# Kernel tuning notes

Hardware: AMD Instinct MI355X
Metric: run time of the kernel (lower is better)

## Reference

```python
import jax, jax.numpy as jnp
import numpy as np

B, OBS, ACT_DIM, C, CTX, H = 128, 512, 7, 100, 128, 512
IN = OBS + 1 + CTX  # states + scalar action component + context = 641


def cont2disc(values, n):
    return jnp.clip(jnp.floor((values + 1.0) / 2.0 * n), 0, n - 1)


def setup_inputs() -> dict:
    key = jax.random.key(0)
    ks = jax.random.split(key, 10)
    def w(k, shape):
        return jax.random.normal(k, shape, dtype=jnp.float32) / np.sqrt(shape[-2])
    return {
        "observations": jax.random.normal(ks[0], (B, OBS), dtype=jnp.float32),
        "actions": jax.random.uniform(ks[1], (B, ACT_DIM), dtype=jnp.float32, minval=-1.0, maxval=1.0),
        # one MLP per action dim (weight_sharing=False): layers IN->H->H->CTX
        "W1": w(ks[2], (ACT_DIM, IN, H)),  "b1": jnp.zeros((ACT_DIM, H), jnp.float32),
        "W2": w(ks[3], (ACT_DIM, H, H)),   "b2": jnp.zeros((ACT_DIM, H), jnp.float32),
        "W3": w(ks[4], (ACT_DIM, H, CTX)), "b3": jnp.zeros((ACT_DIM, CTX), jnp.float32),
        # output_proj = MLP((1,)): single dense CTX->1, no activation
        "Wp": w(ks[5], (CTX, 1)), "bp": jnp.zeros((1,), jnp.float32),
        "compute_lse": 1,
    }


def reference(observations, actions, W1, b1, W2, b2, W3, b3, Wp, bp, compute_lse):
    n = observations.shape[0]
    acts = cont2disc(actions, C)  # [B, ACT_DIM], float component indices
    context = jnp.zeros((n, CTX), observations.dtype)
    comp = jnp.arange(C, dtype=observations.dtype)  # candidate components 0..C-1
    q = jnp.zeros((n, ACT_DIM * C), observations.dtype)

    for i in range(1, ACT_DIM):
        def mlp(x, i=i):  # hidden layers relu, final layer linear
            h = jax.nn.relu(x @ W1[i] + b1[i])
            h = jax.nn.relu(h @ W2[i] + b2[i])
            return h @ W3[i] + b3[i]

        # batched over all num_components candidate actions (replaces the per-j loop)
        xin = jnp.concatenate([
            jnp.broadcast_to(observations[:, None, :], (n, C, OBS)),
            jnp.broadcast_to(comp[None, :, None], (n, C, 1)),
            jnp.broadcast_to(context[:, None, :], (n, C, CTX)),
        ], axis=-1)  # [B, C, IN]
        curr_ctx = mlp(xin) + context[:, None, :]        # [B, C, CTX]
        qv = (curr_ctx @ Wp + bp)[..., 0]                # [B, C]
        q = q.at[:, (i - 1) * C : i * C].set(qv)          # which_qval ordering

        # advance context with the actual (discretized) action
        x = jnp.concatenate([observations, acts[:, i:i + 1], context], axis=-1)
        context = mlp(x) + context

    if compute_lse:
        return jax.scipy.special.logsumexp(q, axis=-1)    # [B]
    return context @ Wp + bp                              # [B, 1]
```

## Files before the change

### kernel.cpp

```cpp
#include <hip/hip_runtime.h>
#include <math.h>

#define BATCH 128
#define ACT 7
#define NC 100
#define CTXD 128
#define HID 512
#define QW 600

typedef __attribute__((ext_vector_type(8))) __bf16 bf16x8;
typedef __attribute__((ext_vector_type(4))) float f32x4;
typedef __attribute__((ext_vector_type(4))) unsigned short u16x4;

__device__ __forceinline__ unsigned short f2bf(float f) {
    union { float f; unsigned int u; } v; v.f = f;
    unsigned int u = v.u;
    return (unsigned short)((u + 0x7fffu + ((u >> 16) & 1u)) >> 16);
}
__device__ __forceinline__ unsigned int pack2bf(float a, float b) {
    unsigned int ua = __float_as_uint(a) + 0x8000u;
    unsigned int ub = __float_as_uint(b) + 0x8000u;
    return (ua >> 16) | (ub & 0xffff0000u);
}

__device__ __forceinline__ void async16(const void* g, void* l) {
    __builtin_amdgcn_global_load_lds(
        (const __attribute__((address_space(1))) unsigned int*)(uintptr_t)g,
        (__attribute__((address_space(3))) unsigned int*)(unsigned int)(uintptr_t)l,
        16, 0, 0);
}

__global__ void prep_kernel(const float* __restrict__ obs, const float* __restrict__ W1,
                            const float* __restrict__ W2, const float* __restrict__ W3,
                            const float* __restrict__ Wp,
                            unsigned short* __restrict__ obs_bf, unsigned short* __restrict__ W1Cbf,
                            unsigned short* __restrict__ W2bf, unsigned short* __restrict__ W3bf,
                            unsigned short* __restrict__ W1AT, unsigned short* __restrict__ W2T,
                            float* __restrict__ vq) {
    const int bidx = blockIdx.x, tid = threadIdx.x;
    if (bidx < 2368) {
        const int e = (bidx * 256 + tid) * 4;
        const float* src; unsigned short* dst;
        if (e < 65536)        { src = obs + e; dst = obs_bf + e; }
        else if (e < 458752)  { int f = e - 65536; int i = f >> 16; int rem = f & 65535;
                                src = W1 + (size_t)(i + 1) * 328192 + 513*512 + rem; dst = W1Cbf + f; }
        else if (e < 2031616) { int f = e - 458752; src = W2 + 262144 + f; dst = W2bf + f; }
        else                  { int f = e - 2031616; src = W3 + 65536 + f; dst = W3bf + f; }
        float4 v = *(const float4*)src;
        u16x4 o; o[0] = f2bf(v.x); o[1] = f2bf(v.y); o[2] = f2bf(v.z); o[3] = f2bf(v.w);
        *(u16x4*)dst = o;
    } else if (bidx < 5440) {
        __shared__ float tile[32][33];
        const int idx = bidx - 2368;
        const int z = idx >> 8, rem = idx & 255;
        const int rb = rem & 15, cb = rem >> 4;
        const float* ip; unsigned short* op;
        if (z < 6) { ip = W1 + (size_t)(z + 1) * 328192; op = W1AT + (size_t)z * 262144; }
        else       { int i = z - 6; ip = W2 + (size_t)(i + 1) * 262144; op = W2T + (size_t)i * 262144; }
        const int r0 = rb * 32, c0 = cb * 32;
        const int tx = tid & 31, ty = tid >> 5;
        #pragma unroll
        for (int j = 0; j < 32; j += 8)
            tile[ty + j][tx] = ip[(size_t)(r0 + ty + j) * 512 + c0 + tx];
        __syncthreads();
        #pragma unroll
        for (int j = 0; j < 32; j += 8)
            op[(size_t)(c0 + ty + j) * 512 + r0 + tx] = f2bf(tile[tx][ty + j]);
    } else {
        const int idx = bidx - 5440;
        const int z = idx >> 1, k = (idx & 1) * 256 + tid;
        const float4* row = (const float4*)(W3 + (size_t)(z + 1) * 65536 + (size_t)k * 128);
        const float4* wp4 = (const float4*)Wp;
        float s = 0.f;
        #pragma unroll 8
        for (int n = 0; n < 32; ++n) {
            float4 a = row[n], w = wp4[n];
            s += a.x*w.x + a.y*w.y + a.z*w.z + a.w*w.w;
        }
        vq[z * 512 + k] = s;
    }
}

__launch_bounds__(256)
__global__ void yobs_kernel(const unsigned short* __restrict__ A,
                            const unsigned short* __restrict__ BtAll,
                            const float* __restrict__ b1,
                            float* __restrict__ Yobs) {
    __shared__ unsigned short As[64*32];
    __shared__ unsigned short Bs[128*32];
    const int m0 = blockIdx.x * 64;
    const int n0 = blockIdx.y * 128;
    const int z  = blockIdx.z;
    const unsigned short* Bt = BtAll + (size_t)z * 262144;
    const int tid = threadIdx.x, lane = tid & 63, wave = tid >> 6;
    const int wm = wave >> 1, wn = wave & 1;
    const int srow = tid >> 2, skc = (tid & 3) * 8;
    const unsigned short* gA  = A  + (size_t)(m0 + srow) * HID + skc;
    const unsigned short* gB0 = Bt + (size_t)(n0 + srow) * HID + skc;
    const unsigned short* gB1 = gB0 + 64 * HID;
    f32x4 acc[2][4] = {};
    for (int k0 = 0; k0 < HID; k0 += 32) {
        async16(gA + k0, As + tid*8);
        async16(gB0 + k0, Bs + tid*8);
        async16(gB1 + k0, Bs + 2048 + tid*8);
        __syncthreads();
        const int q8 = (lane >> 4) * 8, l15 = lane & 15;
        bf16x8 af[2], bfr[4];
        #pragma unroll
        for (int mt = 0; mt < 2; ++mt)
            af[mt] = *(const bf16x8*)(As + (wm*32 + mt*16 + l15) * 32 + q8);
        #pragma unroll
        for (int nt = 0; nt < 4; ++nt)
            bfr[nt] = *(const bf16x8*)(Bs + (wn*64 + nt*16 + l15) * 32 + q8);
        #pragma unroll
        for (int mt = 0; mt < 2; ++mt)
            #pragma unroll
            for (int nt = 0; nt < 4; ++nt)
                acc[mt][nt] = __builtin_amdgcn_mfma_f32_16x16x32_bf16(af[mt], bfr[nt], acc[mt][nt], 0, 0, 0);
        __syncthreads();
    }
    const int colL = wn*64 + (lane & 15);
    #pragma unroll
    for (int nt = 0; nt < 4; ++nt) {
        const int col = n0 + colL + nt*16;
        const float bb = b1[(z + 1) * HID + col];
        #pragma unroll
        for (int mt = 0; mt < 2; ++mt)
            #pragma unroll
            for (int r = 0; r < 4; ++r) {
                const int row = m0 + wm*32 + mt*16 + (lane >> 4)*4 + r;
                Yobs[(size_t)z * 65536 + (size_t)row * HID + col] = acc[mt][nt][r] + bb;
            }
    }
}

__launch_bounds__(1024)
__global__ void chain_kernel(const float* __restrict__ Yobs, const float* __restrict__ W1,
                             const unsigned short* __restrict__ W1Cbf,
                             const unsigned short* __restrict__ W2bf,
                             const unsigned short* __restrict__ W3bf,
                             const float* __restrict__ b2, const float* __restrict__ b3,
                             const float* __restrict__ actions,
                             const float* __restrict__ Wp, const float* __restrict__ bp,
                             float* __restrict__ Y0all, float* __restrict__ QOFF) {
    const int b = blockIdx.x, t = threadIdx.x;
    __shared__ float ctx[128], h1[512], h2s[512];
    __shared__ float part[2048];
    const int pair = t & 255, kq = t >> 8;
    const int pair3 = t & 63, kq3 = t >> 6;
    if (t < 128) ctx[t] = 0.f;
    __syncthreads();
    for (int i = 1; i <= 6; ++i) {
        if (t < 128) part[t] = (ctx[t] + b3[i*128 + t]) * Wp[t];
        __syncthreads();
        if (t < 64) {
            float v = part[t] + part[t + 64];
            #pragma unroll
            for (int o = 32; o > 0; o >>= 1) v += __shfl_down(v, o, 64);
            if (t == 0) QOFF[(i-1)*128 + b] = v + bp[0];
        }
        __syncthreads();
        const float a = actions[b*ACT + i];
        float fj = floorf((a + 1.0f) * 50.0f);
        fj = fminf(fmaxf(fj, 0.0f), 99.0f);
        {
            const unsigned int* wp1 = (const unsigned int*)(W1Cbf + (size_t)(i-1)*65536) + pair;
            float acc0 = 0.f, acc1 = 0.f;
            #pragma unroll 8
            for (int k = kq*32; k < kq*32 + 32; ++k) {
                unsigned int u = wp1[k*256];
                float c = ctx[k];
                acc0 = fmaf(c, __uint_as_float(u << 16), acc0);
                acc1 = fmaf(c, __uint_as_float(u & 0xffff0000u), acc1);
            }
            *(float2*)(&part[kq*512 + 2*pair]) = make_float2(acc0, acc1);
        }
        __syncthreads();
        if (t < 256) {
            const int n2 = 2*t;
            float2 p0 = *(const float2*)(&part[n2]);
            float2 p1 = *(const float2*)(&part[512 + n2]);
            float2 p2 = *(const float2*)(&part[1024 + n2]);
            float2 p3 = *(const float2*)(&part[1536 + n2]);
            float2 yo = *(const float2*)(Yobs + (size_t)(i-1)*65536 + b*512 + n2);
            float y0a = yo.x + p0.x + p1.x + p2.x + p3.x;
            float y0b = yo.y + p0.y + p1.y + p2.y + p3.y;
            *(float2*)(Y0all + (size_t)(i-1)*65536 + b*512 + n2) = make_float2(y0a, y0b);
            const float* w1a = W1 + (size_t)i*328192 + 262144;
            float2 wv = *(const float2*)(w1a + n2);
            h1[n2]   = fmaxf(fmaf(fj, wv.x, y0a), 0.f);
            h1[n2+1] = fmaxf(fmaf(fj, wv.y, y0b), 0.f);
        }
        __syncthreads();
        {
            const unsigned int* wp2 = (const unsigned int*)(W2bf + (size_t)(i-1)*262144) + pair;
            float acc0 = 0.f, acc1 = 0.f;
            #pragma unroll 16
            for (int k = kq*128; k < kq*128 + 128; ++k) {
                unsigned int u = wp2[k*256];
                float hv = h1[k];
                acc0 = fmaf(hv, __uint_as_float(u << 16), acc0);
                acc1 = fmaf(hv, __uint_as_float(u & 0xffff0000u), acc1);
            }
            *(float2*)(&part[kq*512 + 2*pair]) = make_float2(acc0, acc1);
        }
        __syncthreads();
        if (t < 256) {
            const int n2 = 2*t;
            float2 p0 = *(const float2*)(&part[n2]);
            float2 p1 = *(const float2*)(&part[512 + n2]);
            float2 p2 = *(const float2*)(&part[1024 + n2]);
            float2 p3 = *(const float2*)(&part[1536 + n2]);
            float2 bb = *(const float2*)(b2 + i*512 + n2);
            h2s[n2]   = fmaxf(p0.x + p1.x + p2.x + p3.x + bb.x, 0.f);
            h2s[n2+1] = fmaxf(p0.y + p1.y + p2.y + p3.y + bb.y, 0.f);
        }
        __syncthreads();
        {
            const unsigned int* wp3 = (const unsigned int*)(W3bf + (size_t)(i-1)*65536) + pair3;
            float acc0 = 0.f, acc1 = 0.f;
            #pragma unroll 8
            for (int k = kq3*32; k < kq3*32 + 32; ++k) {
                unsigned int u = wp3[k*64];
                float hv = h2s[k];
                acc0 = fmaf(hv, __uint_as_float(u << 16), acc0);
                acc1 = fmaf(hv, __uint_as_float(u & 0xffff0000u), acc1);
            }
            *(float2*)(&part[kq3*128 + 2*pair3]) = make_float2(acc0, acc1);
        }
        __syncthreads();
        if (t < 128) {
            float s = 0.f;
            #pragma unroll
            for (int qg = 0; qg < 16; ++qg) s += part[qg*128 + t];
            ctx[t] = s + b3[i*128 + t] + ctx[t];
        }
        __syncthreads();
    }
}

__global__ void h1all_kernel(const float* __restrict__ Y0all, const float* __restrict__ W1,
                             unsigned short* __restrict__ H1) {
    const int t = blockIdx.x * 256 + threadIdx.x;
    const int row = t >> 6, kc = (t & 63) << 3;
    const int z = row / 12800, rr = row - z * 12800;
    const int b = rr / 100;
    const float c = (float)(rr - b * 100);
    const float* yp = Y0all + (size_t)z*65536 + (size_t)b*512 + kc;
    const float* wp = W1 + (size_t)(z+1)*328192 + 262144 + kc;
    float4 ya = *(const float4*)(yp), yb = *(const float4*)(yp + 4);
    float4 wa = *(const float4*)(wp), wb = *(const float4*)(wp + 4);
    uint4 o;
    o.x = pack2bf(fmaxf(fmaf(c, wa.x, ya.x), 0.f), fmaxf(fmaf(c, wa.y, ya.y), 0.f));
    o.y = pack2bf(fmaxf(fmaf(c, wa.z, ya.z), 0.f), fmaxf(fmaf(c, wa.w, ya.w), 0.f));
    o.z = pack2bf(fmaxf(fmaf(c, wb.x, yb.x), 0.f), fmaxf(fmaf(c, wb.y, yb.y), 0.f));
    o.w = pack2bf(fmaxf(fmaf(c, wb.z, yb.z), 0.f), fmaxf(fmaf(c, wb.w, yb.w), 0.f));
    *(uint4*)(H1 + (size_t)row * 512 + kc) = o;
}

__launch_bounds__(256)
__global__ void gemm2q_kernel(const unsigned short* __restrict__ H1,
                              const unsigned short* __restrict__ W2T,
                              const float* __restrict__ b2,
                              const float* __restrict__ vq, float* __restrict__ qpart) {
    __shared__ unsigned short As[2][4096];
    __shared__ unsigned short Bs[2][4096];
    const int bidx = blockIdx.x;
    const int xcd = bidx & 7, seq = bidx >> 3;
    const int plane = seq & 3;
    const int rt = xcd * 75 + (seq >> 2);
    const int z  = rt / 100;
    const int r0 = rt * 128;
    const int n0 = plane * 128;
    const int tid = threadIdx.x, lane = tid & 63, wave = tid >> 6;
    const int wm = wave >> 1, wn = wave & 1;
    const int srow = tid >> 2, skc = (tid & 3) * 8;
    const int l15 = lane & 15, q8 = (lane >> 4) * 8;
    const unsigned short* gA0 = H1 + (size_t)(r0 + srow)*512 + skc;
    const unsigned short* gA1 = gA0 + 64*512;
    const unsigned short* gB0 = W2T + (size_t)z*262144 + (size_t)(n0 + srow)*512 + skc;
    const unsigned short* gB1 = gB0 + 64*512;
    f32x4 acc[4][4] = {};
    for (int k0 = 0; k0 < 512; k0 += 64) {
        async16(gA0 + k0,      &As[0][tid*8]);
        async16(gA1 + k0,      &As[0][2048 + tid*8]);
        async16(gA0 + k0 + 32, &As[1][tid*8]);
        async16(gA1 + k0 + 32, &As[1][2048 + tid*8]);
        async16(gB0 + k0,      &Bs[0][tid*8]);
        async16(gB1 + k0,      &Bs[0][2048 + tid*8]);
        async16(gB0 + k0 + 32, &Bs[1][tid*8]);
        async16(gB1 + k0 + 32, &Bs[1][2048 + tid*8]);
        __syncthreads();
        #pragma unroll
        for (int h = 0; h < 2; ++h) {
            bf16x8 af[4], bfr[4];
            #pragma unroll
            for (int mt = 0; mt < 4; ++mt)
                af[mt] = *(const bf16x8*)(&As[h][(wm*64 + mt*16 + l15)*32 + q8]);
            #pragma unroll
            for (int nt = 0; nt < 4; ++nt)
                bfr[nt] = *(const bf16x8*)(&Bs[h][(wn*64 + nt*16 + l15)*32 + q8]);
            #pragma unroll
            for (int mt = 0; mt < 4; ++mt)
                #pragma unroll
                for (int nt = 0; nt < 4; ++nt)
                    acc[mt][nt] = __builtin_amdgcn_mfma_f32_16x16x32_bf16(af[mt], bfr[nt], acc[mt][nt], 0, 0, 0);
        }
        __syncthreads();
    }
    float vb[4], bb[4];
    #pragma unroll
    for (int nt = 0; nt < 4; ++nt) {
        const int col = n0 + wn*64 + nt*16 + l15;
        bb[nt] = b2[(z+1)*512 + col];
        vb[nt] = vq[z*512 + col];
    }
    const int plane2 = plane * 2 + wn;
    const int gq = lane >> 4;
    #pragma unroll
    for (int mt = 0; mt < 4; ++mt)
        #pragma unroll
        for (int r = 0; r < 4; ++r) {
            float p = 0.f;
            #pragma unroll
            for (int nt = 0; nt < 4; ++nt)
                p = fmaf(fmaxf(acc[mt][nt][r] + bb[nt], 0.f), vb[nt], p);
            p += __shfl_xor(p, 1, 64);
            p += __shfl_xor(p, 2, 64);
            p += __shfl_xor(p, 4, 64);
            p += __shfl_xor(p, 8, 64);
            if (l15 == 0) {
                const int grow = r0 + wm*64 + mt*16 + gq*4 + r;
                qpart[(size_t)plane2 * 76800 + grow] = p;
            }
        }
}

__global__ void lse_kernel(const float* __restrict__ qpart, const float* __restrict__ QOFF,
                           float* __restrict__ out) {
    __shared__ float red[256];
    __shared__ float qs[QW];
    const int b = blockIdx.x, t = threadIdx.x;
    for (int k = t; k < QW; k += 256) {
        const int z = k / 100, gc = k - z * 100;
        const int grow = z * 12800 + b * 100 + gc;
        float s = QOFF[z * 128 + b];
        #pragma unroll
        for (int p = 0; p < 8; ++p) s += qpart[(size_t)p * 76800 + grow];
        qs[k] = s;
    }
    __syncthreads();
    float m = 0.0f;
    for (int k = t; k < QW; k += 256) m = fmaxf(m, qs[k]);
    red[t] = m; __syncthreads();
    for (int s = 128; s > 0; s >>= 1) { if (t < s) red[t] = fmaxf(red[t], red[t+s]); __syncthreads(); }
    m = red[0]; __syncthreads();
    float sum = 0.0f;
    for (int k = t; k < QW; k += 256) sum += expf(qs[k] - m);
    red[t] = sum; __syncthreads();
    for (int s = 128; s > 0; s >>= 1) { if (t < s) red[t] += red[t+s]; __syncthreads(); }
    if (t == 0) out[b] = logf(red[0] + 100.0f * expf(-m)) + m;
}

extern "C" void kernel_launch(void* const* d_in, const int* in_sizes, int n_in,
                              void* d_out, int out_size, void* d_ws, size_t ws_size,
                              hipStream_t stream) {
    const float* obs     = (const float*)d_in[0];
    const float* actions = (const float*)d_in[1];
    const float* W1      = (const float*)d_in[2];
    const float* b1      = (const float*)d_in[3];
    const float* W2      = (const float*)d_in[4];
    const float* b2      = (const float*)d_in[5];
    const float* W3      = (const float*)d_in[6];
    const float* b3      = (const float*)d_in[7];
    const float* Wp      = (const float*)d_in[8];
    const float* bp      = (const float*)d_in[9];
    float* out = (float*)d_out;
    float* ws  = (float*)d_ws;

    unsigned short* obs_bf = (unsigned short*)(ws);
    unsigned short* W1AT   = (unsigned short*)(ws + 32768);
    unsigned short* W2T    = (unsigned short*)(ws + 819200);
    unsigned short* W1Cbf  = (unsigned short*)(ws + 1605632);
    unsigned short* W2bf   = (unsigned short*)(ws + 1802240);
    unsigned short* W3bf   = (unsigned short*)(ws + 2588672);
    float* Yobs  = ws + 2785280;
    float* Y0all = ws + 3178496;
    float* QOFF  = ws + 3571712;
    float* vq    = ws + 3572736;
    float* qpart = ws + 3575808;
    unsigned short* H1 = (unsigned short*)(ws + 4190208);

    prep_kernel<<<5452, 256, 0, stream>>>(obs, W1, W2, W3, Wp,
                                          obs_bf, W1Cbf, W2bf, W3bf, W1AT, W2T, vq);
    yobs_kernel<<<dim3(2,4,6), 256, 0, stream>>>(obs_bf, W1AT, b1, Yobs);
    chain_kernel<<<BATCH, 1024, 0, stream>>>(Yobs, W1, W1Cbf, W2bf, W3bf, b2, b3, actions, Wp, bp, Y0all, QOFF);
    h1all_kernel<<<19200, 256, 0, stream>>>(Y0all, W1, H1);
    gemm2q_kernel<<<2400, 256, 0, stream>>>(H1, W2T, b2, vq, qpart);
    lse_kernel<<<BATCH, 256, 0, stream>>>(qpart, QOFF, out);
}
```

Measured before the change: 235.7 us.

## Restructure gemm2q into 256x128 tiles with triple-buffered async loads and swizzled LDS

The GEMM2+q-projection kernel now uses 512-thread workgroups computing 256-row by 128-column tiles, so each B tile is reused by more A rows. K-tiles of 64 are staged through a three-deep LDS ring with async global-to-LDS copies issued two stages ahead. Partial vmcnt waits and one barrier per step replace the two full barriers per iteration. LDS columns are XOR-swizzled to avoid bank conflicts, and MFMA sections are wrapped in s_setprio. LDS use grows to about 144KB per block, which limits occupancy to one block per CU, and correctness depends on the hand-written waitcnt counts.

```diff
diff --git a/kernel.cpp b/kernel.cpp
--- a/kernel.cpp
+++ b/kernel.cpp
@@ -258,65 +258,97 @@
     *(uint4*)(H1 + (size_t)row * 512 + kc) = o;
 }
 
-__launch_bounds__(256)
+__launch_bounds__(512)
 __global__ void gemm2q_kernel(const unsigned short* __restrict__ H1,
                               const unsigned short* __restrict__ W2T,
                               const float* __restrict__ b2,
                               const float* __restrict__ vq, float* __restrict__ qpart) {
-    __shared__ unsigned short As[2][4096];
-    __shared__ unsigned short Bs[2][4096];
-    const int bidx = blockIdx.x;
-    const int xcd = bidx & 7, seq = bidx >> 3;
-    const int plane = seq & 3;
-    const int rt = xcd * 75 + (seq >> 2);
-    const int z  = rt / 100;
-    const int r0 = rt * 128;
-    const int n0 = plane * 128;
+    __shared__ __align__(16) unsigned short Ab[3][16384];
+    __shared__ __align__(16) unsigned short Bb[3][8192];
+    const int orig = blockIdx.x;
+    const int wg = (orig & 7) * 150 + (orig >> 3);
+    const int bn = wg & 3, mtile = wg >> 2;
+    const int z  = mtile / 50;
+    const int r0 = mtile * 256;
+    const int n0 = bn * 128;
     const int tid = threadIdx.x, lane = tid & 63, wave = tid >> 6;
     const int wm = wave >> 1, wn = wave & 1;
-    const int srow = tid >> 2, skc = (tid & 3) * 8;
-    const int l15 = lane & 15, q8 = (lane >> 4) * 8;
-    const unsigned short* gA0 = H1 + (size_t)(r0 + srow)*512 + skc;
-    const unsigned short* gA1 = gA0 + 64*512;
-    const unsigned short* gB0 = W2T + (size_t)z*262144 + (size_t)(n0 + srow)*512 + skc;
-    const unsigned short* gB1 = gB0 + 64*512;
+    const int l15 = lane & 15, gq = lane >> 4;
+    const int cb0 = (gq ^ (l15 & 7)) * 8;
+    const int rw = tid >> 3;
+    const int cbx = ((tid & 7) ^ (rw & 7)) * 8;
+    const unsigned short* gA = H1 + (size_t)(r0 + rw) * 512 + cbx;
+    const unsigned short* gB = W2T + (size_t)z * 262144 + (size_t)(n0 + rw) * 512 + cbx;
     f32x4 acc[4][4] = {};
-    for (int k0 = 0; k0 < 512; k0 += 64) {
-        async16(gA0 + k0,      &As[0][tid*8]);
-        async16(gA1 + k0,      &As[0][2048 + tid*8]);
-        async16(gA0 + k0 + 32, &As[1][tid*8]);
-        async16(gA1 + k0 + 32, &As[1][2048 + tid*8]);
-        async16(gB0 + k0,      &Bs[0][tid*8]);
-        async16(gB1 + k0,      &Bs[0][2048 + tid*8]);
-        async16(gB0 + k0 + 32, &Bs[1][tid*8]);
-        async16(gB1 + k0 + 32, &Bs[1][2048 + tid*8]);
-        __syncthreads();
-        #pragma unroll
-        for (int h = 0; h < 2; ++h) {
-            bf16x8 af[4], bfr[4];
-            #pragma unroll
-            for (int mt = 0; mt < 4; ++mt)
-                af[mt] = *(const bf16x8*)(&As[h][(wm*64 + mt*16 + l15)*32 + q8]);
+
+#define STAGE2Q(kt, cbuf) do {                                               \
+    const int k0_ = (kt) * 64;                                               \
+    _Pragma("unroll")                                                        \
+    for (int s = 0; s < 4; ++s)                                              \
+        async16(gA + k0_ + s * 32768, &Ab[cbuf][(s * 512 + tid) * 8]);       \
+    _Pragma("unroll")                                                        \
+    for (int s = 0; s < 2; ++s)                                              \
+        async16(gB + k0_ + s * 32768, &Bb[cbuf][(s * 512 + tid) * 8]);       \
+} while (0)
+
+    STAGE2Q(0, 0);
+    STAGE2Q(1, 1);
+    asm volatile("s_waitcnt vmcnt(6)" ::: "memory");
+    __builtin_amdgcn_sched_barrier(0);
+    __builtin_amdgcn_s_barrier();
+
+    const int arow = (wm * 64 + l15) * 64;
+    const int brow = (wn * 64 + l15) * 64;
+
+    #pragma unroll
+    for (int t = 0; t < 8; ++t) {
+        const int c = t % 3;
+        bf16x8 af[4], bfr[4];
+        #pragma unroll
+        for (int mt = 0; mt < 4; ++mt)
+            af[mt] = *(const bf16x8*)(&Ab[c][arow + mt * 1024 + cb0]);
+        #pragma unroll
+        for (int nt = 0; nt < 4; ++nt)
+            bfr[nt] = *(const bf16x8*)(&Bb[c][brow + nt * 1024 + cb0]);
+        if (t < 6) STAGE2Q(t + 2, (t + 2) % 3);
+        __builtin_amdgcn_s_setprio(1);
+        #pragma unroll
+        for (int mt = 0; mt < 4; ++mt)
             #pragma unroll
             for (int nt = 0; nt < 4; ++nt)
-                bfr[nt] = *(const bf16x8*)(&Bs[h][(wn*64 + nt*16 + l15)*32 + q8]);
-            #pragma unroll
-            for (int mt = 0; mt < 4; ++mt)
-                #pragma unroll
-                for (int nt = 0; nt < 4; ++nt)
-                    acc[mt][nt] = __builtin_amdgcn_mfma_f32_16x16x32_bf16(af[mt], bfr[nt], acc[mt][nt], 0, 0, 0);
-        }
-        __syncthreads();
-    }
-    float vb[4], bb[4];
+                acc[mt][nt] = __builtin_amdgcn_mfma_f32_16x16x32_bf16(af[mt], bfr[nt], acc[mt][nt], 0, 0, 0);
+        __builtin_amdgcn_s_setprio(0);
+        #pragma unroll
+        for (int mt = 0; mt < 4; ++mt)
+            af[mt] = *(const bf16x8*)(&Ab[c][arow + mt * 1024 + (cb0 ^ 32)]);
+        #pragma unroll
+        for (int nt = 0; nt < 4; ++nt)
+            bfr[nt] = *(const bf16x8*)(&Bb[c][brow + nt * 1024 + (cb0 ^ 32)]);
+        __builtin_amdgcn_s_setprio(1);
+        #pragma unroll
+        for (int mt = 0; mt < 4; ++mt)
+            #pragma unroll
+            for (int nt = 0; nt < 4; ++nt)
+                acc[mt][nt] = __builtin_amdgcn_mfma_f32_16x16x32_bf16(af[mt], bfr[nt], acc[mt][nt], 0, 0, 0);
+        __builtin_amdgcn_s_setprio(0);
+        if (t < 7) {
+            asm volatile("s_waitcnt lgkmcnt(0)" ::: "memory");
+            if (t < 6)      asm volatile("s_waitcnt vmcnt(6)" ::: "memory");
+            else            asm volatile("s_waitcnt vmcnt(0)" ::: "memory");
+            __builtin_amdgcn_sched_barrier(0);
+            __builtin_amdgcn_s_barrier();
+        }
+    }
+#undef STAGE2Q
+
+    float vb[4], bbv[4];
     #pragma unroll
     for (int nt = 0; nt < 4; ++nt) {
-        const int col = n0 + wn*64 + nt*16 + l15;
-        bb[nt] = b2[(z+1)*512 + col];
-        vb[nt] = vq[z*512 + col];
-    }
-    const int plane2 = plane * 2 + wn;
-    const int gq = lane >> 4;
+        const int col = n0 + wn * 64 + nt * 16 + l15;
+        bbv[nt] = b2[(z + 1) * 512 + col];
+        vb[nt]  = vq[z * 512 + col];
+    }
+    const int plane2 = bn * 2 + wn;
     #pragma unroll
     for (int mt = 0; mt < 4; ++mt)
         #pragma unroll
@@ -324,13 +356,13 @@
             float p = 0.f;
             #pragma unroll
             for (int nt = 0; nt < 4; ++nt)
-                p = fmaf(fmaxf(acc[mt][nt][r] + bb[nt], 0.f), vb[nt], p);
+                p = fmaf(fmaxf(acc[mt][nt][r] + bbv[nt], 0.f), vb[nt], p);
             p += __shfl_xor(p, 1, 64);
             p += __shfl_xor(p, 2, 64);
             p += __shfl_xor(p, 4, 64);
             p += __shfl_xor(p, 8, 64);
             if (l15 == 0) {
-                const int grow = r0 + wm*64 + mt*16 + gq*4 + r;
+                const int grow = r0 + wm * 64 + mt * 16 + gq * 4 + r;
                 qpart[(size_t)plane2 * 76800 + grow] = p;
             }
         }
@@ -396,6 +428,6 @@
     yobs_kernel<<<dim3(2,4,6), 256, 0, stream>>>(obs_bf, W1AT, b1, Yobs);
     chain_kernel<<<BATCH, 1024, 0, stream>>>(Yobs, W1, W1Cbf, W2bf, W3bf, b2, b3, actions, Wp, bp, Y0all, QOFF);
     h1all_kernel<<<19200, 256, 0, stream>>>(Y0all, W1, H1);
-    gemm2q_kernel<<<2400, 256, 0, stream>>>(H1, W2T, b2, vq, qpart);
+    gemm2q_kernel<<<1200, 512, 0, stream>>>(H1, W2T, b2, vq, qpart);
     lse_kernel<<<BATCH, 256, 0, stream>>>(qpart, QOFF, out);
 }
```

Measured after the change: 225.4 us. 4.4% less time.

## Batch sequential context chain over 16 rows per block using MFMA split-bf16

Applied to the files above, without the earlier changes.

The serial context-advance chain moves from one block per batch row doing scalar FMA GEMVs to 8 blocks, each handling 16 batch rows, with the three layers done as bf16 MFMA matmuls. Activations are split into high and low bf16 halves to keep near-fp32 accuracy, and swizzled LDS layouts are used to avoid bank conflicts. The prep kernel now writes transposed bf16 copies of the W1 context slice and W3 so the chain reuses the already-transposed W2T, which drops the separate bf16 weight copies. The risk is parallelism: only 8 workgroups run the latency-bound chain, versus 128 before.

```diff
diff --git a/kernel.cpp b/kernel.cpp
--- a/kernel.cpp
+++ b/kernel.cpp
@@ -17,6 +17,9 @@
     unsigned int u = v.u;
     return (unsigned short)((u + 0x7fffu + ((u >> 16) & 1u)) >> 16);
 }
+__device__ __forceinline__ float bf2f(unsigned short h) {
+    return __uint_as_float((unsigned int)h << 16);
+}
 __device__ __forceinline__ unsigned int pack2bf(float a, float b) {
     unsigned int ua = __float_as_uint(a) + 0x8000u;
     unsigned int ub = __float_as_uint(b) + 0x8000u;
@@ -33,41 +36,49 @@
 __global__ void prep_kernel(const float* __restrict__ obs, const float* __restrict__ W1,
                             const float* __restrict__ W2, const float* __restrict__ W3,
                             const float* __restrict__ Wp,
-                            unsigned short* __restrict__ obs_bf, unsigned short* __restrict__ W1Cbf,
-                            unsigned short* __restrict__ W2bf, unsigned short* __restrict__ W3bf,
-                            unsigned short* __restrict__ W1AT, unsigned short* __restrict__ W2T,
-                            float* __restrict__ vq) {
+                            unsigned short* __restrict__ obs_bf, unsigned short* __restrict__ W1AT,
+                            unsigned short* __restrict__ W2T, unsigned short* __restrict__ W1CT,
+                            unsigned short* __restrict__ W3T, float* __restrict__ vq) {
     const int bidx = blockIdx.x, tid = threadIdx.x;
-    if (bidx < 2368) {
+    if (bidx < 64) {
         const int e = (bidx * 256 + tid) * 4;
-        const float* src; unsigned short* dst;
-        if (e < 65536)        { src = obs + e; dst = obs_bf + e; }
-        else if (e < 458752)  { int f = e - 65536; int i = f >> 16; int rem = f & 65535;
-                                src = W1 + (size_t)(i + 1) * 328192 + 513*512 + rem; dst = W1Cbf + f; }
-        else if (e < 2031616) { int f = e - 458752; src = W2 + 262144 + f; dst = W2bf + f; }
-        else                  { int f = e - 2031616; src = W3 + 65536 + f; dst = W3bf + f; }
-        float4 v = *(const float4*)src;
+        float4 v = *(const float4*)(obs + e);
         u16x4 o; o[0] = f2bf(v.x); o[1] = f2bf(v.y); o[2] = f2bf(v.z); o[3] = f2bf(v.w);
-        *(u16x4*)dst = o;
-    } else if (bidx < 5440) {
+        *(u16x4*)(obs_bf + e) = o;
+    } else if (bidx < 3904) {
         __shared__ float tile[32][33];
-        const int idx = bidx - 2368;
-        const int z = idx >> 8, rem = idx & 255;
-        const int rb = rem & 15, cb = rem >> 4;
         const float* ip; unsigned short* op;
-        if (z < 6) { ip = W1 + (size_t)(z + 1) * 328192; op = W1AT + (size_t)z * 262144; }
-        else       { int i = z - 6; ip = W2 + (size_t)(i + 1) * 262144; op = W2T + (size_t)i * 262144; }
-        const int r0 = rb * 32, c0 = cb * 32;
+        int src_ld, dst_ld, r0, c0;
+        if (bidx < 3136) {
+            const int idx = bidx - 64;
+            const int z = idx >> 8, rem = idx & 255;
+            const int rb = rem & 15, cb = rem >> 4;
+            if (z < 6) { ip = W1 + (size_t)(z + 1) * 328192; op = W1AT + (size_t)z * 262144; }
+            else       { int i = z - 6; ip = W2 + (size_t)(i + 1) * 262144; op = W2T + (size_t)i * 262144; }
+            src_ld = 512; dst_ld = 512; r0 = rb * 32; c0 = cb * 32;
+        } else if (bidx < 3520) {
+            const int idx = bidx - 3136;
+            const int i = idx >> 6, t = idx & 63;
+            ip = W1 + (size_t)(i + 1) * 328192 + 513 * 512;
+            op = W1CT + (size_t)i * 65536;
+            src_ld = 512; dst_ld = 128; r0 = (t & 3) * 32; c0 = (t >> 2) * 32;
+        } else {
+            const int idx = bidx - 3520;
+            const int i = idx >> 6, t = idx & 63;
+            ip = W3 + (size_t)(i + 1) * 65536;
+            op = W3T + (size_t)i * 65536;
+            src_ld = 128; dst_ld = 512; r0 = (t & 15) * 32; c0 = (t >> 4) * 32;
+        }
         const int tx = tid & 31, ty = tid >> 5;
         #pragma unroll
         for (int j = 0; j < 32; j += 8)
-            tile[ty + j][tx] = ip[(size_t)(r0 + ty + j) * 512 + c0 + tx];
+            tile[ty + j][tx] = ip[(size_t)(r0 + ty + j) * src_ld + c0 + tx];
         __syncthreads();
         #pragma unroll
         for (int j = 0; j < 32; j += 8)
-            op[(size_t)(c0 + ty + j) * 512 + r0 + tx] = f2bf(tile[tx][ty + j]);
+            op[(size_t)(c0 + ty + j) * dst_ld + r0 + tx] = f2bf(tile[tx][ty + j]);
     } else {
-        const int idx = bidx - 5440;
+        const int idx = bidx - 3904;
         const int z = idx >> 1, k = (idx & 1) * 256 + tid;
         const float4* row = (const float4*)(W3 + (size_t)(z + 1) * 65536 + (size_t)k * 128);
         const float4* wp4 = (const float4*)Wp;
@@ -134,106 +145,136 @@
     }
 }
 
-__launch_bounds__(1024)
+__launch_bounds__(512)
 __global__ void chain_kernel(const float* __restrict__ Yobs, const float* __restrict__ W1,
-                             const unsigned short* __restrict__ W1Cbf,
-                             const unsigned short* __restrict__ W2bf,
-                             const unsigned short* __restrict__ W3bf,
+                             const unsigned short* __restrict__ W1CT,
+                             const unsigned short* __restrict__ W2T,
+                             const unsigned short* __restrict__ W3T,
                              const float* __restrict__ b2, const float* __restrict__ b3,
                              const float* __restrict__ actions,
                              const float* __restrict__ Wp, const float* __restrict__ bp,
                              float* __restrict__ Y0all, float* __restrict__ QOFF) {
-    const int b = blockIdx.x, t = threadIdx.x;
-    __shared__ float ctx[128], h1[512], h2s[512];
-    __shared__ float part[2048];
-    const int pair = t & 255, kq = t >> 8;
-    const int pair3 = t & 63, kq3 = t >> 6;
-    if (t < 128) ctx[t] = 0.f;
+    __shared__ unsigned short ctxh[16*128], ctxl[16*128];
+    __shared__ unsigned short Ah[16*512], Al[16*512];
+    __shared__ unsigned short Bh[16*512], Bl[16*512];
+    __shared__ float wps[128];
+    __shared__ float fjs[16];
+    const int b0 = blockIdx.x * 16;
+    const int tid = threadIdx.x, lane = tid & 63, wave = tid >> 6;
+    const int l15 = lane & 15, gq = lane >> 4;
+    for (int t2 = tid; t2 < 2048; t2 += 512) { ctxh[t2] = 0; ctxl[t2] = 0; }
+    if (tid < 128) wps[tid] = Wp[tid];
     __syncthreads();
+
     for (int i = 1; i <= 6; ++i) {
-        if (t < 128) part[t] = (ctx[t] + b3[i*128 + t]) * Wp[t];
-        __syncthreads();
-        if (t < 64) {
-            float v = part[t] + part[t + 64];
-            #pragma unroll
-            for (int o = 32; o > 0; o >>= 1) v += __shfl_down(v, o, 64);
-            if (t == 0) QOFF[(i-1)*128 + b] = v + bp[0];
-        }
-        __syncthreads();
-        const float a = actions[b*ACT + i];
-        float fj = floorf((a + 1.0f) * 50.0f);
-        fj = fminf(fmaxf(fj, 0.0f), 99.0f);
+        if (tid < 16) {
+            float a = actions[(b0 + tid) * ACT + i];
+            float fj = floorf((a + 1.0f) * 50.0f);
+            fjs[tid] = fminf(fmaxf(fj, 0.0f), 99.0f);
+        }
         {
-            const unsigned int* wp1 = (const unsigned int*)(W1Cbf + (size_t)(i-1)*65536) + pair;
-            float acc0 = 0.f, acc1 = 0.f;
-            #pragma unroll 8
-            for (int k = kq*32; k < kq*32 + 32; ++k) {
-                unsigned int u = wp1[k*256];
-                float c = ctx[k];
-                acc0 = fmaf(c, __uint_as_float(u << 16), acc0);
-                acc1 = fmaf(c, __uint_as_float(u & 0xffff0000u), acc1);
-            }
-            *(float2*)(&part[kq*512 + 2*pair]) = make_float2(acc0, acc1);
-        }
-        __syncthreads();
-        if (t < 256) {
-            const int n2 = 2*t;
-            float2 p0 = *(const float2*)(&part[n2]);
-            float2 p1 = *(const float2*)(&part[512 + n2]);
-            float2 p2 = *(const float2*)(&part[1024 + n2]);
-            float2 p3 = *(const float2*)(&part[1536 + n2]);
-            float2 yo = *(const float2*)(Yobs + (size_t)(i-1)*65536 + b*512 + n2);
-            float y0a = yo.x + p0.x + p1.x + p2.x + p3.x;
-            float y0b = yo.y + p0.y + p1.y + p2.y + p3.y;
-            *(float2*)(Y0all + (size_t)(i-1)*65536 + b*512 + n2) = make_float2(y0a, y0b);
-            const float* w1a = W1 + (size_t)i*328192 + 262144;
-            float2 wv = *(const float2*)(w1a + n2);
-            h1[n2]   = fmaxf(fmaf(fj, wv.x, y0a), 0.f);
-            h1[n2+1] = fmaxf(fmaf(fj, wv.y, y0b), 0.f);
-        }
-        __syncthreads();
+            const int bl = wave * 2 + (lane >> 5);
+            const int c0 = (lane & 31) * 4;
+            float p = 0.f;
+            #pragma unroll
+            for (int j = 0; j < 4; ++j) {
+                const int c = c0 + j;
+                const int ad = bl * 128 + (((c >> 3) ^ (bl & 7)) << 3) + (c & 7);
+                const float cv = bf2f(ctxh[ad]) + bf2f(ctxl[ad]);
+                p += (cv + b3[i * 128 + c]) * wps[c];
+            }
+            p += __shfl_xor(p, 1, 64);  p += __shfl_xor(p, 2, 64);
+            p += __shfl_xor(p, 4, 64);  p += __shfl_xor(p, 8, 64);
+            p += __shfl_xor(p, 16, 64);
+            if ((lane & 31) == 0) QOFF[(i - 1) * 128 + b0 + bl] = p + bp[0];
+        }
+        __syncthreads();
+
+        const float* w1a = W1 + (size_t)i * 328192 + 262144;
+        #pragma unroll
+        for (int j = 0; j < 4; ++j) {
+            const int n0c = (wave + 8 * j) * 16;
+            f32x4 acc = {};
+            const unsigned short* wt = W1CT + (size_t)(i - 1) * 65536 + (size_t)(n0c + l15) * 128;
+            #pragma unroll
+            for (int kt = 0; kt < 4; ++kt) {
+                const int su = ((kt * 4 + gq) ^ (l15 & 7)) * 8;
+                bf16x8 ah = *(const bf16x8*)(ctxh + l15 * 128 + su);
+                bf16x8 al = *(const bf16x8*)(ctxl + l15 * 128 + su);
+                bf16x8 bb = *(const bf16x8*)(wt + kt * 32 + gq * 8);
+                acc = __builtin_amdgcn_mfma_f32_16x16x32_bf16(ah, bb, acc, 0, 0, 0);
+                acc = __builtin_amdgcn_mfma_f32_16x16x32_bf16(al, bb, acc, 0, 0, 0);
+            }
+            const int col = n0c + l15;
+            const float wcol = w1a[col];
+            #pragma unroll
+            for (int r = 0; r < 4; ++r) {
+                const int row = gq * 4 + r;
+                const size_t go = (size_t)(i - 1) * 65536 + (size_t)(b0 + row) * 512 + col;
+                const float y0 = acc[r] + Yobs[go];
+                Y0all[go] = y0;
+                const float h = fmaxf(fmaf(fjs[row], wcol, y0), 0.f);
+                const unsigned short hh = f2bf(h);
+                const unsigned short hl = f2bf(h - bf2f(hh));
+                const int ad = row * 512 + (((col >> 3) ^ (row & 7)) << 3) + (col & 7);
+                Ah[ad] = hh; Al[ad] = hl;
+            }
+        }
+        __syncthreads();
+
+        #pragma unroll
+        for (int j = 0; j < 4; ++j) {
+            const int n0c = (wave + 8 * j) * 16;
+            f32x4 acc = {};
+            const unsigned short* wt = W2T + (size_t)(i - 1) * 262144 + (size_t)(n0c + l15) * 512;
+            #pragma unroll
+            for (int kt = 0; kt < 16; ++kt) {
+                const int su = ((kt * 4 + gq) ^ (l15 & 7)) * 8;
+                bf16x8 ah = *(const bf16x8*)(Ah + l15 * 512 + su);
+                bf16x8 al = *(const bf16x8*)(Al + l15 * 512 + su);
+                bf16x8 bb = *(const bf16x8*)(wt + kt * 32 + gq * 8);
+                acc = __builtin_amdgcn_mfma_f32_16x16x32_bf16(ah, bb, acc, 0, 0, 0);
+                acc = __builtin_amdgcn_mfma_f32_16x16x32_bf16(al, bb, acc, 0, 0, 0);
+            }
+            const int col = n0c + l15;
+            const float bcol = b2[i * 512 + col];
+            #pragma unroll
+            for (int r = 0; r < 4; ++r) {
+                const int row = gq * 4 + r;
+                const float h = fmaxf(acc[r] + bcol, 0.f);
+                const unsigned short hh = f2bf(h);
+                const unsigned short hl = f2bf(h - bf2f(hh));
+                const int ad = row * 512 + (((col >> 3) ^ (row & 7)) << 3) + (col & 7);
+                Bh[ad] = hh; Bl[ad] = hl;
+            }
+        }
+        __syncthreads();
+
         {
-            const unsigned int* wp2 = (const unsigned int*)(W2bf + (size_t)(i-1)*262144) + pair;
-            float acc0 = 0.f, acc1 = 0.f;
-            #pragma unroll 16
-            for (int k = kq*128; k < kq*128 + 128; ++k) {
-                unsigned int u = wp2[k*256];
-                float hv = h1[k];
-                acc0 = fmaf(hv, __uint_as_float(u << 16), acc0);
-                acc1 = fmaf(hv, __uint_as_float(u & 0xffff0000u), acc1);
-            }
-            *(float2*)(&part[kq*512 + 2*pair]) = make_float2(acc0, acc1);
-        }
-        __syncthreads();
-        if (t < 256) {
-            const int n2 = 2*t;
-            float2 p0 = *(const float2*)(&part[n2]);
-            float2 p1 = *(const float2*)(&part[512 + n2]);
-            float2 p2 = *(const float2*)(&part[1024 + n2]);
-            float2 p3 = *(const float2*)(&part[1536 + n2]);
-            float2 bb = *(const float2*)(b2 + i*512 + n2);
-            h2s[n2]   = fmaxf(p0.x + p1.x + p2.x + p3.x + bb.x, 0.f);
-            h2s[n2+1] = fmaxf(p0.y + p1.y + p2.y + p3.y + bb.y, 0.f);
-        }
-        __syncthreads();
-        {
-            const unsigned int* wp3 = (const unsigned int*)(W3bf + (size_t)(i-1)*65536) + pair3;
-            float acc0 = 0.f, acc1 = 0.f;
-            #pragma unroll 8
-            for (int k = kq3*32; k < kq3*32 + 32; ++k) {
-                unsigned int u = wp3[k*64];
-                float hv = h2s[k];
-                acc0 = fmaf(hv, __uint_as_float(u << 16), acc0);
-                acc1 = fmaf(hv, __uint_as_float(u & 0xffff0000u), acc1);
-            }
-            *(float2*)(&part[kq3*128 + 2*pair3]) = make_float2(acc0, acc1);
-        }
-        __syncthreads();
-        if (t < 128) {
-            float s = 0.f;
-            #pragma unroll
-            for (int qg = 0; qg < 16; ++qg) s += part[qg*128 + t];
-            ctx[t] = s + b3[i*128 + t] + ctx[t];
+            const int n0c = wave * 16;
+            f32x4 acc = {};
+            const unsigned short* wt = W3T + (size_t)(i - 1) * 65536 + (size_t)(n0c + l15) * 512;
+            #pragma unroll
+            for (int kt = 0; kt < 16; ++kt) {
+                const int su = ((kt * 4 + gq) ^ (l15 & 7)) * 8;
+                bf16x8 ah = *(const bf16x8*)(Bh + l15 * 512 + su);
+                bf16x8 al = *(const bf16x8*)(Bl + l15 * 512 + su);
+                bf16x8 bb = *(const bf16x8*)(wt + kt * 32 + gq * 8);
+                acc = __builtin_amdgcn_mfma_f32_16x16x32_bf16(ah, bb, acc, 0, 0, 0);
+                acc = __builtin_amdgcn_mfma_f32_16x16x32_bf16(al, bb, acc, 0, 0, 0);
+            }
+            const int col = n0c + l15;
+            const float b3c = b3[i * 128 + col];
+            #pragma unroll
+            for (int r = 0; r < 4; ++r) {
+                const int row = gq * 4 + r;
+                const int ad = row * 128 + (((col >> 3) ^ (row & 7)) << 3) + (col & 7);
+                const float co = bf2f(ctxh[ad]) + bf2f(ctxl[ad]);
+                const float cn = acc[r] + b3c + co;
+                const unsigned short ch = f2bf(cn);
+                ctxh[ad] = ch;
+                ctxl[ad] = f2bf(cn - bf2f(ch));
+            }
         }
         __syncthreads();
     }
@@ -381,20 +422,19 @@
     unsigned short* obs_bf = (unsigned short*)(ws);
     unsigned short* W1AT   = (unsigned short*)(ws + 32768);
     unsigned short* W2T    = (unsigned short*)(ws + 819200);
-    unsigned short* W1Cbf  = (unsigned short*)(ws + 1605632);
-    unsigned short* W2bf   = (unsigned short*)(ws + 1802240);
-    unsigned short* W3bf   = (unsigned short*)(ws + 2588672);
-    float* Yobs  = ws + 2785280;
-    float* Y0all = ws + 3178496;
-    float* QOFF  = ws + 3571712;
-    float* vq    = ws + 3572736;
-    float* qpart = ws + 3575808;
-    unsigned short* H1 = (unsigned short*)(ws + 4190208);
-
-    prep_kernel<<<5452, 256, 0, stream>>>(obs, W1, W2, W3, Wp,
-                                          obs_bf, W1Cbf, W2bf, W3bf, W1AT, W2T, vq);
+    unsigned short* W1CT   = (unsigned short*)(ws + 1605632);
+    unsigned short* W3T    = (unsigned short*)(ws + 1802240);
+    float* Yobs  = ws + 1998848;
+    float* Y0all = ws + 2392064;
+    float* QOFF  = ws + 2785280;
+    float* vq    = ws + 2786304;
+    float* qpart = ws + 2789376;
+    unsigned short* H1 = (unsigned short*)(ws + 3403776);
+
+    prep_kernel<<<3916, 256, 0, stream>>>(obs, W1, W2, W3, Wp,
+                                          obs_bf, W1AT, W2T, W1CT, W3T, vq);
     yobs_kernel<<<dim3(2,4,6), 256, 0, stream>>>(obs_bf, W1AT, b1, Yobs);
-    chain_kernel<<<BATCH, 1024, 0, stream>>>(Yobs, W1, W1Cbf, W2bf, W3bf, b2, b3, actions, Wp, bp, Y0all, QOFF);
+    chain_kernel<<<8, 512, 0, stream>>>(Yobs, W1, W1CT, W2T, W3T, b2, b3, actions, Wp, bp, Y0all, QOFF);
     h1all_kernel<<<19200, 256, 0, stream>>>(Y0all, W1, H1);
     gemm2q_kernel<<<2400, 256, 0, stream>>>(H1, W2T, b2, vq, qpart);
     lse_kernel<<<BATCH, 256, 0, stream>>>(qpart, QOFF, out);
```

Result: slower. 375.0 us (+59.1%).

## Pipeline chain kernel weight loads through a 4-deep async LDS ring buffer

Applied to the files above, without the earlier changes.

The sequential chain kernel now streams the bf16 W1C/W2/W3 weight slices into a four-slot shared-memory ring with asynchronous global-to-LDS loads. It prefetches two chunks ahead, and even prefetches the next layer's first chunks during the reductions. Barriers are replaced by custom waitcnt+s_barrier macros so loads overlap the FMA work. This aims to hide the global memory latency of per-element strided weight reads, at the cost of 128KB of LDS. The large LDS footprint may limit occupancy, and the hand-tuned vmcnt counts are fragile.

```diff
diff --git a/kernel.cpp b/kernel.cpp
--- a/kernel.cpp
+++ b/kernel.cpp
@@ -29,6 +29,23 @@
         (__attribute__((address_space(3))) unsigned int*)(unsigned int)(uintptr_t)l,
         16, 0, 0);
 }
+
+#define BAR_LG() do { __builtin_amdgcn_sched_barrier(0); \
+    asm volatile("s_waitcnt lgkmcnt(0)" ::: "memory"); \
+    __builtin_amdgcn_s_barrier(); \
+    __builtin_amdgcn_sched_barrier(0); } while (0)
+#define BAR_VL() do { __builtin_amdgcn_sched_barrier(0); \
+    asm volatile("s_waitcnt vmcnt(2) lgkmcnt(0)" ::: "memory"); \
+    __builtin_amdgcn_s_barrier(); \
+    __builtin_amdgcn_sched_barrier(0); } while (0)
+#define BAR_V2() do { __builtin_amdgcn_sched_barrier(0); \
+    asm volatile("s_waitcnt vmcnt(2)" ::: "memory"); \
+    __builtin_amdgcn_s_barrier(); \
+    __builtin_amdgcn_sched_barrier(0); } while (0)
+#define BAR_V0() do { __builtin_amdgcn_sched_barrier(0); \
+    asm volatile("s_waitcnt vmcnt(0)" ::: "memory"); \
+    __builtin_amdgcn_s_barrier(); \
+    __builtin_amdgcn_sched_barrier(0); } while (0)
 
 __global__ void prep_kernel(const float* __restrict__ obs, const float* __restrict__ W1,
                             const float* __restrict__ W2, const float* __restrict__ W3,
@@ -146,36 +163,89 @@
     const int b = blockIdx.x, t = threadIdx.x;
     __shared__ float ctx[128], h1[512], h2s[512];
     __shared__ float part[2048];
+    __shared__ __align__(16) unsigned short wbuf[4][16384];
     const int pair = t & 255, kq = t >> 8;
     const int pair3 = t & 63, kq3 = t >> 6;
+
+#define STAGEW(srcsh, bufi) do {                                   \
+    const unsigned short* s_ = (srcsh);                            \
+    async16(s_ + (size_t)t * 8,          &wbuf[bufi][t * 8]);      \
+    async16(s_ + (size_t)(1024 + t) * 8, &wbuf[bufi][(1024 + t) * 8]); \
+} while (0)
+
+#define L1_CHUNK(c) do {                                           \
+    const unsigned int* wb_ = (const unsigned int*)wbuf[(c) & 3];  \
+    _Pragma("unroll")                                              \
+    for (int kk = 0; kk < 8; ++kk) {                               \
+        const int kl = kq * 8 + kk;                                \
+        unsigned int u = wb_[kl * 256 + pair];                     \
+        float cv = ctx[(c) * 32 + kl];                             \
+        acc0 = fmaf(cv, __uint_as_float(u << 16), acc0);           \
+        acc1 = fmaf(cv, __uint_as_float(u & 0xffff0000u), acc1);   \
+    } } while (0)
+
+#define L2_CHUNK(c) do {                                           \
+    const unsigned int* wb_ = (const unsigned int*)wbuf[(c) & 3];  \
+    _Pragma("unroll")                                              \
+    for (int kk = 0; kk < 8; ++kk) {                               \
+        const int kl = kq * 8 + kk;                                \
+        unsigned int u = wb_[kl * 256 + pair];                     \
+        float hv = h1[(c) * 32 + kl];                              \
+        acc0 = fmaf(hv, __uint_as_float(u << 16), acc0);           \
+        acc1 = fmaf(hv, __uint_as_float(u & 0xffff0000u), acc1);   \
+    } } while (0)
+
+#define L3_CHUNK(c) do {                                           \
+    const unsigned int* wb_ = (const unsigned int*)wbuf[(c) & 3];  \
+    _Pragma("unroll")                                              \
+    for (int kk = 0; kk < 8; ++kk) {                               \
+        const int kl = kq3 * 8 + kk;                               \
+        unsigned int u = wb_[kl * 64 + pair3];                     \
+        float hv = h2s[(c) * 128 + kl];                            \
+        acc0 = fmaf(hv, __uint_as_float(u << 16), acc0);           \
+        acc1 = fmaf(hv, __uint_as_float(u & 0xffff0000u), acc1);   \
+    } } while (0)
+
+    STAGEW(W1Cbf, 0);
+    STAGEW(W1Cbf + 16384, 1);
     if (t < 128) ctx[t] = 0.f;
-    __syncthreads();
+    BAR_LG();
+
     for (int i = 1; i <= 6; ++i) {
+        const unsigned short* w1src = W1Cbf + (size_t)(i - 1) * 65536;
+        const unsigned short* w2src = W2bf + (size_t)(i - 1) * 262144;
+        const unsigned short* w3src = W3bf + (size_t)(i - 1) * 65536;
+
         if (t < 128) part[t] = (ctx[t] + b3[i*128 + t]) * Wp[t];
-        __syncthreads();
+        BAR_LG();
         if (t < 64) {
             float v = part[t] + part[t + 64];
             #pragma unroll
             for (int o = 32; o > 0; o >>= 1) v += __shfl_down(v, o, 64);
             if (t == 0) QOFF[(i-1)*128 + b] = v + bp[0];
         }
-        __syncthreads();
+        BAR_VL();
         const float a = actions[b*ACT + i];
         float fj = floorf((a + 1.0f) * 50.0f);
         fj = fminf(fmaxf(fj, 0.0f), 99.0f);
+
         {
-            const unsigned int* wp1 = (const unsigned int*)(W1Cbf + (size_t)(i-1)*65536) + pair;
             float acc0 = 0.f, acc1 = 0.f;
-            #pragma unroll 8
-            for (int k = kq*32; k < kq*32 + 32; ++k) {
-                unsigned int u = wp1[k*256];
-                float c = ctx[k];
-                acc0 = fmaf(c, __uint_as_float(u << 16), acc0);
-                acc1 = fmaf(c, __uint_as_float(u & 0xffff0000u), acc1);
-            }
+            STAGEW(w1src + 2*16384, 2);
+            L1_CHUNK(0);
+            BAR_V2();
+            STAGEW(w1src + 3*16384, 3);
+            L1_CHUNK(1);
+            BAR_V2();
+            L1_CHUNK(2);
+            BAR_V0();
+            L1_CHUNK(3);
             *(float2*)(&part[kq*512 + 2*pair]) = make_float2(acc0, acc1);
         }
-        __syncthreads();
+        STAGEW(w2src, 0);
+        STAGEW(w2src + 16384, 1);
+        BAR_LG();
+
         if (t < 256) {
             const int n2 = 2*t;
             float2 p0 = *(const float2*)(&part[n2]);
@@ -191,20 +261,22 @@
             h1[n2]   = fmaxf(fmaf(fj, wv.x, y0a), 0.f);
             h1[n2+1] = fmaxf(fmaf(fj, wv.y, y0b), 0.f);
         }
-        __syncthreads();
+        BAR_VL();
+
         {
-            const unsigned int* wp2 = (const unsigned int*)(W2bf + (size_t)(i-1)*262144) + pair;
             float acc0 = 0.f, acc1 = 0.f;
-            #pragma unroll 16
-            for (int k = kq*128; k < kq*128 + 128; ++k) {
-                unsigned int u = wp2[k*256];
-                float hv = h1[k];
-                acc0 = fmaf(hv, __uint_as_float(u << 16), acc0);
-                acc1 = fmaf(hv, __uint_as_float(u & 0xffff0000u), acc1);
+            #pragma unroll
+            for (int c = 0; c < 16; ++c) {
+                if (c + 2 < 16) STAGEW(w2src + (size_t)(c + 2) * 16384, (c + 2) & 3);
+                L2_CHUNK(c);
+                if (c < 15) { if (c + 2 < 16) BAR_V2(); else BAR_V0(); }
             }
             *(float2*)(&part[kq*512 + 2*pair]) = make_float2(acc0, acc1);
         }
-        __syncthreads();
+        STAGEW(w3src, 0);
+        STAGEW(w3src + 16384, 1);
+        BAR_LG();
+
         if (t < 256) {
             const int n2 = 2*t;
             float2 p0 = *(const float2*)(&part[n2]);
@@ -215,28 +287,40 @@
             h2s[n2]   = fmaxf(p0.x + p1.x + p2.x + p3.x + bb.x, 0.f);
             h2s[n2+1] = fmaxf(p0.y + p1.y + p2.y + p3.y + bb.y, 0.f);
         }
-        __syncthreads();
+        BAR_VL();
+
         {
-            const unsigned int* wp3 = (const unsigned int*)(W3bf + (size_t)(i-1)*65536) + pair3;
             float acc0 = 0.f, acc1 = 0.f;
-            #pragma unroll 8
-            for (int k = kq3*32; k < kq3*32 + 32; ++k) {
-                unsigned int u = wp3[k*64];
-                float hv = h2s[k];
-                acc0 = fmaf(hv, __uint_as_float(u << 16), acc0);
-                acc1 = fmaf(hv, __uint_as_float(u & 0xffff0000u), acc1);
-            }
+            STAGEW(w3src + 2*16384, 2);
+            L3_CHUNK(0);
+            BAR_V2();
+            STAGEW(w3src + 3*16384, 3);
+            L3_CHUNK(1);
+            BAR_V2();
+            L3_CHUNK(2);
+            BAR_V0();
+            L3_CHUNK(3);
             *(float2*)(&part[kq3*128 + 2*pair3]) = make_float2(acc0, acc1);
         }
-        __syncthreads();
+        if (i < 6) {
+            const unsigned short* wn = W1Cbf + (size_t)i * 65536;
+            STAGEW(wn, 0);
+            STAGEW(wn + 16384, 1);
+        }
+        BAR_LG();
+
         if (t < 128) {
             float s = 0.f;
             #pragma unroll
             for (int qg = 0; qg < 16; ++qg) s += part[qg*128 + t];
             ctx[t] = s + b3[i*128 + t] + ctx[t];
         }
-        __syncthreads();
-    }
+        BAR_LG();
+    }
+#undef STAGEW
+#undef L1_CHUNK
+#undef L2_CHUNK
+#undef L3_CHUNK
 }
 
 __global__ void h1all_kernel(const float* __restrict__ Y0all, const float* __restrict__ W1,
```

Result: slower. 241.3 us (+2.3%).
